# Optimization experiments

Measured on AMD Instinct MI355X. Metric: run time of the kernel, lower is better.

## Reference

```python
import jax, jax.numpy as jnp
import numpy as np
from jax import lax

B, T, R, D = 32, 128, 9, 512


def conv2d(x, w, b):
    # x: (N,C,H,W), w: (O,I,kh,kw)
    y = lax.conv_general_dilated(x, w, (1, 1), 'VALID', dimension_numbers=('NCHW', 'OIHW', 'NCHW'))
    return y + b[None, :, None, None]


def pad1(x):
    return jnp.pad(x, ((0, 0), (0, 0), (1, 1), (1, 1)))


def maxpool2(x):
    return lax.reduce_window(x, -jnp.inf, lax.max, (1, 1, 2, 2), (1, 1, 2, 2), 'VALID')


def f2f_similarity(q, t, qm, tm):
    # q,t: (B,T,R,D). Region-pairwise sims then Chamfer: max over target regions p (axis 3), mean over query regions o (axis 2).
    sim = jnp.einsum('biok,bjpk->biopj', q, t)   # (B,T,R,R,T) large intermediate
    sim = jnp.mean(jnp.max(sim, axis=3), axis=2)  # (B,T,T)
    smask = qm[:, :, None] * tm[:, None, :]       # (B,T,T)
    sim = jnp.where(smask > 0, sim, 0.0)
    return sim, smask


def visil_head(sim, mask, w1, b1, w2, b2, w3, b3, wf, bf):
    # ViSiL VideoComperator: zeropad1+conv3x3+relu+maxpool2 (x2), zeropad1+conv3x3+relu, 1x1 conv
    x = sim[:, None]   # (N,1,T,T)
    m = mask[:, None]
    x = maxpool2(jax.nn.relu(conv2d(pad1(x), w1, b1)))
    m = maxpool2(m)
    x = maxpool2(jax.nn.relu(conv2d(pad1(x), w2, b2)))
    m = maxpool2(m)
    x = jax.nn.relu(conv2d(pad1(x), w3, b3))
    x = conv2d(x, wf, bf)   # 1x1 conv -> 1 channel
    return x[:, 0], m[:, 0]


def chamfer_v2v(s, m):
    # masked Chamfer: max over axis 2, masked mean over axis 1
    s = jnp.where(m > 0, s, -jnp.inf)
    s = jnp.max(s, axis=2)
    mm = jnp.max(m, axis=2)
    s = jnp.where(mm > 0, s, 0.0)
    return jnp.sum(s, axis=1) / jnp.sum(mm, axis=1)


def setup_inputs():
    key = jax.random.key(0)
    ks = jax.random.split(key, 8)
    return {
        'anchors': jax.random.normal(ks[0], (B, T, R, D), jnp.float32),
        'positives': jax.random.normal(ks[1], (B, T, R, D), jnp.float32),
        'negatives': jax.random.normal(ks[2], (B, T, R, D), jnp.float32),
        'anchors_masks': jnp.ones((B, T), jnp.float32),
        'positive_masks': jnp.ones((B, T), jnp.float32),
        'negative_masks': jnp.ones((B, T), jnp.float32),
        'w1': jax.random.normal(ks[3], (32, 1, 3, 3), jnp.float32) * 0.05,
        'b1': jnp.zeros((32,), jnp.float32),
        'w2': jax.random.normal(ks[4], (64, 32, 3, 3), jnp.float32) * 0.05,
        'b2': jnp.zeros((64,), jnp.float32),
        'w3': jax.random.normal(ks[5], (128, 64, 3, 3), jnp.float32) * 0.05,
        'b3': jnp.zeros((128,), jnp.float32),
        'wf': jax.random.normal(ks[6], (1, 128, 1, 1), jnp.float32) * 0.05,
        'bf': jnp.zeros((1,), jnp.float32),
    }


def reference(anchors, positives, negatives, anchors_masks, positive_masks, negative_masks, w1, b1, w2, b2, w3, b3, wf, bf):
    pos_sim, pos_mask = f2f_similarity(anchors, positives, anchors_masks, positive_masks)
    neg_sim, neg_mask = f2f_similarity(anchors, negatives, anchors_masks, negative_masks)
    sim = jnp.concatenate([pos_sim, neg_sim], 0)
    smask = jnp.concatenate([pos_mask, neg_mask], 0)
    sim, smask = visil_head(sim, smask, w1, b1, w2, b2, w3, b3, wf, bf)
    # SimilarityRegularizationLoss(min_val=-1, max_val=1)
    loss = jnp.sum(jax.nn.relu(-1.0 - sim)) + jnp.sum(jax.nn.relu(sim - 1.0))
    sim = jnp.clip(sim, -1.0, 1.0)  # Hardtanh
    v2v = chamfer_v2v(sim, smask)   # (2B,)
    pos_pair, neg_pair = jnp.split(v2v[:, None], 2, axis=0)
    return pos_pair, neg_pair, loss
```

## Files before the change

### kernel.cpp

```cpp
#include <hip/hip_runtime.h>
#include <math.h>

#define BTRD (128*9*512)

typedef _Float16 half8 __attribute__((ext_vector_type(8)));
typedef float f32x4 __attribute__((ext_vector_type(4)));

__global__ __launch_bounds__(256) void prep_kernel(
    const float* __restrict__ P, const float* __restrict__ Nn,
    _Float16* __restrict__ Pf, _Float16* __restrict__ Nf,
    const float* __restrict__ w2, const float* __restrict__ w3,
    _Float16* __restrict__ w2t, _Float16* __restrict__ w3t)
{
  int bid = blockIdx.x;
  if (bid < 18432) {
    int which = bid / 9216;
    const float* in = which == 0 ? P : Nn;
    _Float16* out = which == 0 ? Pf : Nf;
    int idx = (bid - which * 9216) * 256 + threadIdx.x;
    const float4* in4 = (const float4*)in;
    float4 a = in4[idx * 2], c = in4[idx * 2 + 1];
    half8 h = { (_Float16)a.x, (_Float16)a.y, (_Float16)a.z, (_Float16)a.w,
                (_Float16)c.x, (_Float16)c.y, (_Float16)c.z, (_Float16)c.w };
    ((half8*)out)[idx] = h;
  } else {
    int idx = (bid - 18432) * 256 + threadIdx.x;
    if (idx < 18432) {
      int tap = idx >> 11, oc = (idx >> 5) & 63, ic = idx & 31;
      w2t[idx] = (_Float16)w2[(oc * 32 + ic) * 9 + tap];
    } else if (idx < 18432 + 73728) {
      int j = idx - 18432;
      int tap = j >> 13, oc = (j >> 6) & 127, ic = j & 63;
      w3t[j] = (_Float16)w3[(oc * 64 + ic) * 9 + tap];
    }
  }
}

template<int O, int OB>
__device__ __forceinline__ void sim_run(
    const float* __restrict__ Q32, const _Float16* __restrict__ T,
    _Float16* __restrict__ lds, int i0, int tid, int jhalf,
    int pb, int b, int g,
    const float* __restrict__ qm, const float* __restrict__ pm,
    const float* __restrict__ nm, float* __restrict__ simout)
{
  int lane = tid & 63;
  int lrow = lane & 15, lk8 = lane >> 4;
  _Float16* tb0 = lds + 73728;
  _Float16* tb1 = lds + 73728 + 4096;

  {
    const float* qb = Q32 + ((size_t)(i0 * 9) << 9);
    for (int it = 0; it < 36; it++) {
      int c = it * 256 + tid;
      int r = c >> 6, sp = c & 63;
      const float* src = qb + ((size_t)r << 9) + (sp << 3);
      float4 a = *(const float4*)src;
      float4 cc = *(const float4*)(src + 4);
      half8 h = { (_Float16)a.x, (_Float16)a.y, (_Float16)a.z, (_Float16)a.w,
                  (_Float16)cc.x, (_Float16)cc.y, (_Float16)cc.z, (_Float16)cc.w };
      *(half8*)&lds[r * 512 + ((sp ^ (r & 7)) << 3)] = h;
    }
  }

  int c0 = tid, c1 = tid + 256;
  int j0c = c0 >> 2, sp0 = c0 & 3;
  int j1c = c1 >> 2, sp1 = c1 & 3;
  const _Float16* tg0 = T + ((size_t)(j0c * 9) << 9) + (sp0 << 3);
  const _Float16* tg1 = T + ((size_t)(j1c * 9) << 9) + (sp1 << 3);
  int ld0 = j0c * 32 + ((sp0 ^ ((j0c >> 1) & 3)) << 3);
  int ld1 = j1c * 32 + ((sp1 ^ ((j1c >> 1) & 3)) << 3);

  half8 st[4][2];

#define T_ISSUE(SET, S) do {                                              \
    int _s = (S);                                                         \
    int _p = _s >> 4; _p = _p > 8 ? 8 : _p;                               \
    int _off = (_p << 9) + ((_s & 15) << 5);                              \
    st[SET][0] = *(const half8*)(tg0 + _off);                             \
    st[SET][1] = *(const half8*)(tg1 + _off);                             \
  } while (0)

#define T_WRITE(SET, PAR) do {                                            \
    _Float16* _buf = (PAR) ? tb1 : tb0;                                   \
    *(half8*)&_buf[ld0] = st[SET][0];                                     \
    *(half8*)&_buf[ld1] = st[SET][1];                                     \
  } while (0)

  T_ISSUE(0, 0);
  T_ISSUE(1, 1);
  T_ISSUE(2, 2);
  T_WRITE(0, 0);
  asm volatile("s_waitcnt lgkmcnt(0)" ::: "memory");
  __builtin_amdgcn_s_barrier();
  __builtin_amdgcn_sched_barrier(0);

  f32x4 acc[O][4], mx[O][4];
#pragma unroll
  for (int oo = 0; oo < O; oo++)
#pragma unroll
    for (int jt = 0; jt < 4; jt++) {
      acc[oo][jt] = (f32x4){0.f, 0.f, 0.f, 0.f};
      mx[oo][jt] = (f32x4){-INFINITY, -INFINITY, -INFINITY, -INFINITY};
    }

  for (int p = 0; p < 9; p++) {
#pragma unroll
    for (int kc = 0; kc < 16; kc++) {
      int s = p * 16 + kc;
      T_ISSUE((kc + 3) & 3, s + 3);
      T_WRITE((kc + 1) & 3, (kc + 1) & 1);

      const _Float16* cur = (kc & 1) ? tb1 : tb0;
      half8 bfr[4];
#pragma unroll
      for (int jt = 0; jt < 4; jt++) {
        int j = jhalf * 64 + jt * 16 + lrow;
        bfr[jt] = *(const half8*)&cur[j * 32 + ((lk8 ^ ((j >> 1) & 3)) << 3)];
      }
#pragma unroll
      for (int oo = 0; oo < O; oo++) {
        int r = lrow * 9 + OB + oo;
        half8 afr = *(const half8*)&lds[r * 512 + ((((kc << 2) + lk8) ^ (r & 7)) << 3)];
#pragma unroll
        for (int jt = 0; jt < 4; jt++)
          acc[oo][jt] = __builtin_amdgcn_mfma_f32_16x16x32_f16(afr, bfr[jt], acc[oo][jt], 0, 0, 0);
      }

      if (kc == 15) {
#pragma unroll
        for (int oo = 0; oo < O; oo++)
#pragma unroll
          for (int jt = 0; jt < 4; jt++) {
#pragma unroll
            for (int e = 0; e < 4; e++)
              mx[oo][jt][e] = fmaxf(mx[oo][jt][e], acc[oo][jt][e]);
            acc[oo][jt] = (f32x4){0.f, 0.f, 0.f, 0.f};
          }
      }
      asm volatile("s_waitcnt lgkmcnt(0)" ::: "memory");
      __builtin_amdgcn_s_barrier();
      __builtin_amdgcn_sched_barrier(0);
    }
  }
#undef T_ISSUE
#undef T_WRITE

  f32x4 ps[4];
#pragma unroll
  for (int jt = 0; jt < 4; jt++) {
    ps[jt] = mx[0][jt];
#pragma unroll
    for (int oo = 1; oo < O; oo++) ps[jt] += mx[oo][jt];
  }

  float* ex = (float*)(lds + 73728);
  if (OB != 0) {
#pragma unroll
    for (int jt = 0; jt < 4; jt++)
      *(f32x4*)&ex[((jt * 2 + jhalf) * 64 + lane) * 4] = ps[jt];
  }
  __syncthreads();
  if (OB == 0) {
    const float* tm = (g ? nm : pm) + b * 128;
    const float* qmv = qm + b * 128;
    const float inv9 = 1.0f / 9.0f;
#pragma unroll
    for (int jt = 0; jt < 4; jt++) {
      ps[jt] += *(const f32x4*)&ex[((jt * 2 + jhalf) * 64 + lane) * 4];
      int j = jhalf * 64 + jt * 16 + lrow;
      float tmv = tm[j];
#pragma unroll
      for (int e = 0; e < 4; e++) {
        int i = i0 + (lk8 << 2) + e;
        float m = qmv[i] * tmv;
        simout[((size_t)pb << 14) + (i << 7) + j] = (m > 0.f) ? ps[jt][e] * inv9 : 0.f;
      }
    }
  }
}

__global__ __launch_bounds__(256, 1) void sim_mfma_kernel(
    const float* __restrict__ A32, const _Float16* __restrict__ Pf,
    const _Float16* __restrict__ Nf,
    const float* __restrict__ qm, const float* __restrict__ pm,
    const float* __restrict__ nm, float* __restrict__ simout)
{
  __shared__ _Float16 lds[81920];

  int n = blockIdx.x;
  int xcd = n & 7, slot = n >> 3;
  int pb = xcd * 8 + (slot >> 3);
  int ib = slot & 7;
  int b = pb & 31, g = pb >> 5;
  const float* Q32 = A32 + (size_t)b * BTRD;
  const _Float16* T = (g ? Nf : Pf) + (size_t)b * BTRD;
  int i0 = ib * 16;

  int tid = threadIdx.x;
  int w = tid >> 6;
  int jhalf = w & 1;
  if ((w >> 1) == 0)
    sim_run<5, 0>(Q32, T, lds, i0, tid, jhalf, pb, b, g, qm, pm, nm, simout);
  else
    sim_run<4, 5>(Q32, T, lds, i0, tid, jhalf, pb, b, g, qm, pm, nm, simout);
}

__global__ __launch_bounds__(256) void conv1_kernel(
    const float* __restrict__ sim, const float* __restrict__ w1,
    const float* __restrict__ b1, _Float16* __restrict__ x1)
{
  __shared__ float w_s[288];
  __shared__ float b_s[32];
  int tid = threadIdx.x;
  for (int e = tid; e < 288; e += 256) w_s[e] = w1[e];
  if (tid < 32) b_s[tid] = b1[tid];
  __syncthreads();

  int idx = blockIdx.x * 256 + tid;
  int x = idx & 63, y = (idx >> 6) & 63, b2 = idx >> 12;
  const float* sb = sim + (size_t)b2 * 16384;

  float patch[4][4];
#pragma unroll
  for (int r = 0; r < 4; r++) {
    int Y = 2 * y - 1 + r;
#pragma unroll
    for (int c = 0; c < 4; c++) {
      int X = 2 * x - 1 + c;
      patch[r][c] = (Y >= 0 && Y < 128 && X >= 0 && X < 128) ? sb[Y * 128 + X] : 0.f;
    }
  }

  _Float16 vout[32];
#pragma unroll
  for (int oc = 0; oc < 32; oc++) {
    float c00 = 0, c01 = 0, c10 = 0, c11 = 0;
#pragma unroll
    for (int tap = 0; tap < 9; tap++) {
      int dy = tap / 3, dx = tap - dy * 3;
      float w = w_s[oc * 9 + tap];
      c00 = fmaf(w, patch[dy][dx], c00);
      c01 = fmaf(w, patch[dy][dx + 1], c01);
      c10 = fmaf(w, patch[dy + 1][dx], c10);
      c11 = fmaf(w, patch[dy + 1][dx + 1], c11);
    }
    float v = fmaxf(fmaxf(c00, c01), fmaxf(c10, c11)) + b_s[oc];
    vout[oc] = (_Float16)fmaxf(v, 0.f);
  }
  _Float16* dst = x1 + (((size_t)b2 * 64 + y) * 64 + x) * 32;
#pragma unroll
  for (int q = 0; q < 4; q++)
    *(half8*)(dst + q * 8) = *(half8*)&vout[q * 8];
}

__global__ __launch_bounds__(256, 2) void conv2_mfma(
    const _Float16* __restrict__ x1, const _Float16* __restrict__ w2t,
    const float* __restrict__ bb, _Float16* __restrict__ x2)
{
  __shared__ _Float16 in_s[4 * 6 * 66 * 8];
  __shared__ _Float16 w_s[9 * 64 * 40];
  __shared__ _Float16 pool_s[4][32 * 32];

  int b2 = blockIdx.y, ystrip = blockIdx.x;
  int y0 = ystrip * 4;
  int tid = threadIdx.x;
  int w = tid >> 6, lane = tid & 63;
  int wyp = w >> 1, wn = w & 1;
  int lrow = lane & 15, lk8 = lane >> 4;

  {
    int px = tid >> 2, seg = tid & 3;
    const _Float16* base = x1 + ((size_t)b2 * 64) * 64 * 32;
    for (int rr = 0; rr < 6; rr++) {
      int yy = y0 - 1 + rr;
      half8 v = {};
      if (yy >= 0 && yy < 64) v = *(const half8*)(base + ((size_t)yy * 64 + px) * 32 + seg * 8);
      *(half8*)&in_s[((seg * 6 + rr) * 66 + px + 1) * 8] = v;
    }
    if (tid < 48) {
      int pr = tid >> 1, side = tid & 1;
      *(half8*)&in_s[(pr * 66 + side * 65) * 8] = (half8){};
    }
  }
  for (int e = tid; e < 2304; e += 256)
    *(half8*)&w_s[(e >> 2) * 40 + (e & 3) * 8] = *(const half8*)&w2t[e * 8];
  __syncthreads();

  f32x4 acc[2][4][2];
#pragma unroll
  for (int yr = 0; yr < 2; yr++)
#pragma unroll
    for (int xt = 0; xt < 4; xt++)
#pragma unroll
      for (int nt = 0; nt < 2; nt++)
        acc[yr][xt][nt] = (f32x4){0.f, 0.f, 0.f, 0.f};

#pragma unroll
  for (int tap = 0; tap < 9; tap++) {
    int dy = tap / 3, dx = tap - dy * 3;
    half8 bfr[2];
#pragma unroll
    for (int nt = 0; nt < 2; nt++)
      bfr[nt] = *(const half8*)&w_s[(tap * 64 + wn * 32 + nt * 16 + lrow) * 40 + lk8 * 8];
#pragma unroll
    for (int yr = 0; yr < 2; yr++) {
      int rr = 2 * wyp + yr + dy;
#pragma unroll
      for (int xt = 0; xt < 4; xt++) {
        half8 afr = *(const half8*)&in_s[((lk8 * 6 + rr) * 66 + xt * 16 + lrow + dx) * 8];
#pragma unroll
        for (int nt = 0; nt < 2; nt++)
          acc[yr][xt][nt] = __builtin_amdgcn_mfma_f32_16x16x32_f16(afr, bfr[nt], acc[yr][xt][nt], 0, 0, 0);
      }
    }
  }

  float bbv[2] = { bb[wn * 32 + lrow], bb[wn * 32 + 16 + lrow] };
#pragma unroll
  for (int nt = 0; nt < 2; nt++)
#pragma unroll
    for (int xt = 0; xt < 4; xt++)
#pragma unroll
      for (int pe = 0; pe < 2; pe++) {
        float m = fmaxf(fmaxf(acc[0][xt][nt][2 * pe], acc[0][xt][nt][2 * pe + 1]),
                        fmaxf(acc[1][xt][nt][2 * pe], acc[1][xt][nt][2 * pe + 1]));
        float v = fmaxf(m + bbv[nt], 0.f);
        int px = xt * 8 + lk8 * 2 + pe;
        pool_s[w][px * 32 + nt * 16 + lrow] = (_Float16)v;
      }
  __syncthreads();

  {
    int py = ystrip * 2 + wyp;
    int px = lane & 31, half = lane >> 5;
    const _Float16* srcp = &pool_s[w][px * 32 + half * 16];
    _Float16* dst = x2 + (((size_t)b2 * 32 + py) * 32 + px) * 64 + wn * 32 + half * 16;
    *(half8*)dst = *(const half8*)srcp;
    *(half8*)(dst + 8) = *(const half8*)(srcp + 8);
  }
}

__global__ __launch_bounds__(256, 2) void conv3_mfma(
    const _Float16* __restrict__ x2, const _Float16* __restrict__ w3t,
    const float* __restrict__ b3, const float* __restrict__ wf,
    const float* __restrict__ bf, float* __restrict__ shead)
{
  __shared__ _Float16 in_s[8 * 6 * 34 * 8];
  __shared__ _Float16 w_s[9 * 32 * 72];

  int b2 = blockIdx.y, ystrip = blockIdx.x;
  int y0 = ystrip * 4;
  int tid = threadIdx.x, w = tid >> 6, lane = tid & 63;
  int lrow = lane & 15, lk8 = lane >> 4;

  {
    int px = tid >> 3, seg = tid & 7;
    const _Float16* base = x2 + ((size_t)b2 * 32) * 32 * 64;
    for (int rr = 0; rr < 6; rr++) {
      int yy = y0 - 1 + rr;
      half8 v = {};
      if (yy >= 0 && yy < 32) v = *(const half8*)(base + ((size_t)yy * 32 + px) * 64 + seg * 8);
      *(half8*)&in_s[((seg * 6 + rr) * 34 + px + 1) * 8] = v;
    }
    if (tid < 96) {
      int pr = tid >> 1, side = tid & 1;
      *(half8*)&in_s[(pr * 34 + side * 33) * 8] = (half8){};
    }
  }

  f32x4 spart[2];
  spart[0] = (f32x4){0.f, 0.f, 0.f, 0.f};
  spart[1] = (f32x4){0.f, 0.f, 0.f, 0.f};
  int y = y0 + w;

  for (int og = 0; og < 4; og++) {
    __syncthreads();
    for (int e = tid; e < 2304; e += 256) {
      int s = e & 7, o = (e >> 3) & 31, tap = e >> 8;
      *(half8*)&w_s[(tap * 32 + o) * 72 + s * 8] =
          *(const half8*)&w3t[((size_t)(tap * 128 + og * 32 + o)) * 64 + s * 8];
    }
    __syncthreads();

    f32x4 acc[2][2];
#pragma unroll
    for (int mt = 0; mt < 2; mt++)
#pragma unroll
      for (int nt = 0; nt < 2; nt++)
        acc[mt][nt] = (f32x4){0.f, 0.f, 0.f, 0.f};

#pragma unroll
    for (int tap = 0; tap < 9; tap++) {
      int dy = tap / 3, dx = tap - dy * 3;
#pragma unroll
      for (int kc = 0; kc < 2; kc++) {
        half8 bfr[2];
#pragma unroll
        for (int nt = 0; nt < 2; nt++)
          bfr[nt] = *(const half8*)&w_s[(tap * 32 + nt * 16 + lrow) * 72 + kc * 32 + lk8 * 8];
#pragma unroll
        for (int mt = 0; mt < 2; mt++) {
          half8 afr = *(const half8*)&in_s[(((kc * 4 + lk8) * 6 + w + dy) * 34 + mt * 16 + lrow + dx) * 8];
#pragma unroll
          for (int nt = 0; nt < 2; nt++)
            acc[mt][nt] = __builtin_amdgcn_mfma_f32_16x16x32_f16(afr, bfr[nt], acc[mt][nt], 0, 0, 0);
        }
      }
    }

#pragma unroll
    for (int nt = 0; nt < 2; nt++) {
      int oc = og * 32 + nt * 16 + lrow;
      float b3v = b3[oc], wfv = wf[oc];
#pragma unroll
      for (int mt = 0; mt < 2; mt++)
#pragma unroll
        for (int e = 0; e < 4; e++)
          spart[mt][e] = fmaf(fmaxf(acc[mt][nt][e] + b3v, 0.f), wfv, spart[mt][e]);
    }
  }

#pragma unroll
  for (int mt = 0; mt < 2; mt++)
#pragma unroll
    for (int e = 0; e < 4; e++) {
      float v = spart[mt][e];
      v += __shfl_xor(v, 1); v += __shfl_xor(v, 2);
      v += __shfl_xor(v, 4); v += __shfl_xor(v, 8);
      spart[mt][e] = v;
    }
  if (lrow == 0) {
    float bfv = bf[0];
#pragma unroll
    for (int mt = 0; mt < 2; mt++)
#pragma unroll
      for (int e = 0; e < 4; e++) {
        int x = mt * 16 + lk8 * 4 + e;
        shead[(size_t)b2 * 1024 + y * 32 + x] = spart[mt][e] + bfv;
      }
  }
}

__global__ __launch_bounds__(256) void head_final_kernel(
    const float* __restrict__ shead, const float* __restrict__ qm,
    const float* __restrict__ pm, const float* __restrict__ nm,
    float* __restrict__ out, float* __restrict__ loss_ws)
{
  int b2 = blockIdx.x, b = b2 & 31, g = b2 >> 5;
  const float* qmv = qm + b * 128;
  const float* tmv = (g ? nm : pm) + b * 128;

  __shared__ float mq4[32], mt4[32];
  __shared__ float red[256];
  __shared__ float rowv[32], rowm[32];

  int tid = threadIdx.x;
  if (tid < 32) {
    float a = qmv[tid * 4];
    a = fmaxf(a, qmv[tid * 4 + 1]); a = fmaxf(a, qmv[tid * 4 + 2]); a = fmaxf(a, qmv[tid * 4 + 3]);
    mq4[tid] = a;
    float c = tmv[tid * 4];
    c = fmaxf(c, tmv[tid * 4 + 1]); c = fmaxf(c, tmv[tid * 4 + 2]); c = fmaxf(c, tmv[tid * 4 + 3]);
    mt4[tid] = c;
  }
  __syncthreads();

  const float* s = shead + (size_t)b2 * 1024;
  float lp = 0.f;
#pragma unroll
  for (int r = 0; r < 4; r++) {
    float v = s[tid + 256 * r];
    lp += fmaxf(-1.f - v, 0.f) + fmaxf(v - 1.f, 0.f);
  }
  red[tid] = lp;
  __syncthreads();
  for (int off = 128; off; off >>= 1) {
    if (tid < off) red[tid] += red[tid + off];
    __syncthreads();
  }
  if (tid == 0) loss_ws[b2] = red[0];

  if (tid < 32) {
    int y = tid;
    float mqy = mq4[y];
    float rmax = -INFINITY, mm = 0.f;
    for (int x = 0; x < 32; x++) {
      float m = mqy * mt4[x];
      mm = fmaxf(mm, m);
      float v = s[y * 32 + x];
      v = fminf(fmaxf(v, -1.f), 1.f);
      rmax = fmaxf(rmax, m > 0.f ? v : -INFINITY);
    }
    rowv[y] = (mm > 0.f) ? rmax : 0.f;
    rowm[y] = mm;
  }
  __syncthreads();
  if (tid == 0) {
    float ss = 0.f, sm = 0.f;
    for (int y = 0; y < 32; y++) { ss += rowv[y]; sm += rowm[y]; }
    out[b2] = ss / sm;
  }
}

__global__ void loss_sum_kernel(const float* __restrict__ loss_ws, float* __restrict__ out)
{
  float v = loss_ws[threadIdx.x];
#pragma unroll
  for (int off = 32; off >= 1; off >>= 1) v += __shfl_down(v, off);
  if (threadIdx.x == 0) out[64] = v;
}

extern "C" void kernel_launch(void* const* d_in, const int* in_sizes, int n_in,
                              void* d_out, int out_size, void* d_ws, size_t ws_size,
                              hipStream_t stream)
{
  (void)in_sizes; (void)n_in; (void)out_size; (void)ws_size;
  const float* A   = (const float*)d_in[0];
  const float* P   = (const float*)d_in[1];
  const float* Nn  = (const float*)d_in[2];
  const float* qm  = (const float*)d_in[3];
  const float* pm  = (const float*)d_in[4];
  const float* nm  = (const float*)d_in[5];
  const float* w1  = (const float*)d_in[6];
  const float* b1  = (const float*)d_in[7];
  const float* w2  = (const float*)d_in[8];
  const float* b2w = (const float*)d_in[9];
  const float* w3  = (const float*)d_in[10];
  const float* b3  = (const float*)d_in[11];
  const float* wf  = (const float*)d_in[12];
  const float* bf  = (const float*)d_in[13];
  float* out = (float*)d_out;

  const size_t F16SZ = (size_t)BTRD * 32 * sizeof(_Float16);
  char* ws = (char*)d_ws;
  _Float16* Pf = (_Float16*)(ws);
  _Float16* Nf = (_Float16*)(ws + F16SZ);
  char* ws2 = ws + 2 * F16SZ;
  float*     sim   = (float*)(ws2);
  _Float16*  x1    = (_Float16*)(ws2 + (4u << 20));
  _Float16*  x2    = (_Float16*)(ws2 + (20u << 20));
  float*     shead = (float*)(ws2 + (28u << 20));
  _Float16*  w2t   = (_Float16*)(ws2 + (29u << 20));
  _Float16*  w3t   = (_Float16*)(ws2 + (29u << 20) + (256u << 10));
  float*     lws   = (float*)(ws2 + (30u << 20));

  prep_kernel<<<18792, 256, 0, stream>>>(P, Nn, Pf, Nf, w2, w3, w2t, w3t);

  sim_mfma_kernel<<<512, 256, 0, stream>>>(A, Pf, Nf, qm, pm, nm, sim);
  conv1_kernel<<<1024, 256, 0, stream>>>(sim, w1, b1, x1);
  conv2_mfma<<<dim3(16, 64), 256, 0, stream>>>(x1, w2t, b2w, x2);
  conv3_mfma<<<dim3(8, 64), 256, 0, stream>>>(x2, w3t, b3, wf, bf, shead);
  head_final_kernel<<<64, 256, 0, stream>>>(shead, qm, pm, nm, out, lws);
  loss_sum_kernel<<<1, 64, 0, stream>>>(lws, out);
}
```

Before: 208.5 us.

## Share anchor tile across positive and negative passes, load target fragments directly

The similarity kernel now launches one block per (batch, query tile) with 512 threads. Each block converts the anchor tile to fp16 in LDS once and reuses it for both the positive and negative targets, instead of one block per target. Target fragments are loaded straight from global memory into registers with a small software prefetch ring, which removes the LDS staging buffers and the per-step barriers. This halves anchor conversion and LDS fill work and drops synchronisation, but it halves the grid to 256 blocks and relies on uncoalesced direct global reads of the target data.

```diff
diff --git a/kernel.cpp b/kernel.cpp
--- a/kernel.cpp
+++ b/kernel.cpp
@@ -38,21 +38,20 @@
 
 template<int O, int OB>
 __device__ __forceinline__ void sim_run(
-    const float* __restrict__ Q32, const _Float16* __restrict__ T,
-    _Float16* __restrict__ lds, int i0, int tid, int jhalf,
-    int pb, int b, int g,
+    const float* __restrict__ Q32, const _Float16* __restrict__ TP,
+    const _Float16* __restrict__ TN,
+    _Float16* __restrict__ lds, int i0, int tid, int jq, int b,
     const float* __restrict__ qm, const float* __restrict__ pm,
     const float* __restrict__ nm, float* __restrict__ simout)
 {
   int lane = tid & 63;
   int lrow = lane & 15, lk8 = lane >> 4;
-  _Float16* tb0 = lds + 73728;
-  _Float16* tb1 = lds + 73728 + 4096;
 
   {
     const float* qb = Q32 + ((size_t)(i0 * 9) << 9);
-    for (int it = 0; it < 36; it++) {
-      int c = it * 256 + tid;
+#pragma unroll
+    for (int it = 0; it < 18; it++) {
+      int c = it * 512 + tid;
       int r = c >> 6, sp = c & 63;
       const float* src = qb + ((size_t)r << 9) + (sp << 3);
       float4 a = *(const float4*)src;
@@ -62,148 +61,123 @@
       *(half8*)&lds[r * 512 + ((sp ^ (r & 7)) << 3)] = h;
     }
   }
-
-  int c0 = tid, c1 = tid + 256;
-  int j0c = c0 >> 2, sp0 = c0 & 3;
-  int j1c = c1 >> 2, sp1 = c1 & 3;
-  const _Float16* tg0 = T + ((size_t)(j0c * 9) << 9) + (sp0 << 3);
-  const _Float16* tg1 = T + ((size_t)(j1c * 9) << 9) + (sp1 << 3);
-  int ld0 = j0c * 32 + ((sp0 ^ ((j0c >> 1) & 3)) << 3);
-  int ld1 = j1c * 32 + ((sp1 ^ ((j1c >> 1) & 3)) << 3);
-
-  half8 st[4][2];
-
-#define T_ISSUE(SET, S) do {                                              \
-    int _s = (S);                                                         \
-    int _p = _s >> 4; _p = _p > 8 ? 8 : _p;                               \
-    int _off = (_p << 9) + ((_s & 15) << 5);                              \
-    st[SET][0] = *(const half8*)(tg0 + _off);                             \
-    st[SET][1] = *(const half8*)(tg1 + _off);                             \
-  } while (0)
-
-#define T_WRITE(SET, PAR) do {                                            \
-    _Float16* _buf = (PAR) ? tb1 : tb0;                                   \
-    *(half8*)&_buf[ld0] = st[SET][0];                                     \
-    *(half8*)&_buf[ld1] = st[SET][1];                                     \
-  } while (0)
-
-  T_ISSUE(0, 0);
-  T_ISSUE(1, 1);
-  T_ISSUE(2, 2);
-  T_WRITE(0, 0);
-  asm volatile("s_waitcnt lgkmcnt(0)" ::: "memory");
-  __builtin_amdgcn_s_barrier();
-  __builtin_amdgcn_sched_barrier(0);
-
-  f32x4 acc[O][4], mx[O][4];
-#pragma unroll
-  for (int oo = 0; oo < O; oo++)
-#pragma unroll
-    for (int jt = 0; jt < 4; jt++) {
-      acc[oo][jt] = (f32x4){0.f, 0.f, 0.f, 0.f};
-      mx[oo][jt] = (f32x4){-INFINITY, -INFINITY, -INFINITY, -INFINITY};
-    }
-
-  for (int p = 0; p < 9; p++) {
-#pragma unroll
-    for (int kc = 0; kc < 16; kc++) {
-      int s = p * 16 + kc;
-      T_ISSUE((kc + 3) & 3, s + 3);
-      T_WRITE((kc + 1) & 3, (kc + 1) & 1);
-
-      const _Float16* cur = (kc & 1) ? tb1 : tb0;
-      half8 bfr[4];
-#pragma unroll
-      for (int jt = 0; jt < 4; jt++) {
-        int j = jhalf * 64 + jt * 16 + lrow;
-        bfr[jt] = *(const half8*)&cur[j * 32 + ((lk8 ^ ((j >> 1) & 3)) << 3)];
-      }
-#pragma unroll
-      for (int oo = 0; oo < O; oo++) {
-        int r = lrow * 9 + OB + oo;
-        half8 afr = *(const half8*)&lds[r * 512 + ((((kc << 2) + lk8) ^ (r & 7)) << 3)];
-#pragma unroll
-        for (int jt = 0; jt < 4; jt++)
-          acc[oo][jt] = __builtin_amdgcn_mfma_f32_16x16x32_f16(afr, bfr[jt], acc[oo][jt], 0, 0, 0);
-      }
-
-      if (kc == 15) {
-#pragma unroll
-        for (int oo = 0; oo < O; oo++)
-#pragma unroll
-          for (int jt = 0; jt < 4; jt++) {
-#pragma unroll
-            for (int e = 0; e < 4; e++)
-              mx[oo][jt][e] = fmaxf(mx[oo][jt][e], acc[oo][jt][e]);
-            acc[oo][jt] = (f32x4){0.f, 0.f, 0.f, 0.f};
-          }
-      }
-      asm volatile("s_waitcnt lgkmcnt(0)" ::: "memory");
-      __builtin_amdgcn_s_barrier();
-      __builtin_amdgcn_sched_barrier(0);
-    }
-  }
-#undef T_ISSUE
-#undef T_WRITE
-
-  f32x4 ps[4];
-#pragma unroll
-  for (int jt = 0; jt < 4; jt++) {
-    ps[jt] = mx[0][jt];
-#pragma unroll
-    for (int oo = 1; oo < O; oo++) ps[jt] += mx[oo][jt];
-  }
+  __syncthreads();
 
   float* ex = (float*)(lds + 73728);
-  if (OB != 0) {
-#pragma unroll
-    for (int jt = 0; jt < 4; jt++)
-      *(f32x4*)&ex[((jt * 2 + jhalf) * 64 + lane) * 4] = ps[jt];
-  }
-  __syncthreads();
-  if (OB == 0) {
-    const float* tm = (g ? nm : pm) + b * 128;
-    const float* qmv = qm + b * 128;
-    const float inv9 = 1.0f / 9.0f;
-#pragma unroll
-    for (int jt = 0; jt < 4; jt++) {
-      ps[jt] += *(const f32x4*)&ex[((jt * 2 + jhalf) * 64 + lane) * 4];
-      int j = jhalf * 64 + jt * 16 + lrow;
-      float tmv = tm[j];
-#pragma unroll
-      for (int e = 0; e < 4; e++) {
-        int i = i0 + (lk8 << 2) + e;
-        float m = qmv[i] * tmv;
-        simout[((size_t)pb << 14) + (i << 7) + j] = (m > 0.f) ? ps[jt][e] * inv9 : 0.f;
-      }
-    }
-  }
-}
-
-__global__ __launch_bounds__(256, 1) void sim_mfma_kernel(
+  const float* qmv = qm + b * 128;
+  const float inv9 = 1.0f / 9.0f;
+
+  for (int tsel = 0; tsel < 2; ++tsel) {
+    const _Float16* T = tsel ? TN : TP;
+    const _Float16* tg0 = T + (size_t)(jq * 32 + lrow) * 4608 + (lk8 << 3);
+    const _Float16* tg1 = tg0 + (size_t)16 * 4608;
+
+    half8 Bb[4][2];
+    f32x4 acc[O][2], mx[O][2];
+#pragma unroll
+    for (int oo = 0; oo < O; oo++)
+#pragma unroll
+      for (int jt = 0; jt < 2; jt++) {
+        acc[oo][jt] = (f32x4){0.f, 0.f, 0.f, 0.f};
+        mx[oo][jt] = (f32x4){-INFINITY, -INFINITY, -INFINITY, -INFINITY};
+      }
+
+#define B_ISSUE(SET, S) do {                                              \
+      int _s = (S);                                                       \
+      int _p = _s >> 4; if (_p > 8) _p = 8;                               \
+      int _off = (_p << 9) + ((_s & 15) << 5);                            \
+      Bb[SET][0] = *(const half8*)(tg0 + _off);                           \
+      Bb[SET][1] = *(const half8*)(tg1 + _off);                           \
+    } while (0)
+
+    B_ISSUE(0, 0);
+    B_ISSUE(1, 1);
+
+    for (int p = 0; p < 9; ++p) {
+#pragma unroll
+      for (int kc = 0; kc < 16; ++kc) {
+        int s = p * 16 + kc;
+        B_ISSUE((kc + 2) & 3, s + 2);
+#pragma unroll
+        for (int oo = 0; oo < O; ++oo) {
+          int r = lrow * 9 + OB + oo;
+          half8 afr = *(const half8*)&lds[r * 512 + ((((kc << 2) + lk8) ^ (r & 7)) << 3)];
+          acc[oo][0] = __builtin_amdgcn_mfma_f32_16x16x32_f16(afr, Bb[kc & 3][0], acc[oo][0], 0, 0, 0);
+          acc[oo][1] = __builtin_amdgcn_mfma_f32_16x16x32_f16(afr, Bb[kc & 3][1], acc[oo][1], 0, 0, 0);
+        }
+        if (kc == 15) {
+#pragma unroll
+          for (int oo = 0; oo < O; oo++)
+#pragma unroll
+            for (int jt = 0; jt < 2; jt++) {
+#pragma unroll
+              for (int e = 0; e < 4; e++)
+                mx[oo][jt][e] = fmaxf(mx[oo][jt][e], acc[oo][jt][e]);
+              acc[oo][jt] = (f32x4){0.f, 0.f, 0.f, 0.f};
+            }
+        }
+      }
+    }
+#undef B_ISSUE
+
+    f32x4 ps[2];
+#pragma unroll
+    for (int jt = 0; jt < 2; jt++) {
+      ps[jt] = mx[0][jt];
+#pragma unroll
+      for (int oo = 1; oo < O; oo++) ps[jt] += mx[oo][jt];
+    }
+
+    if (OB != 0) {
+#pragma unroll
+      for (int jt = 0; jt < 2; jt++)
+        *(f32x4*)&ex[((jq * 64 + lane) * 2 + jt) * 4] = ps[jt];
+    }
+    __syncthreads();
+    if (OB == 0) {
+      const float* tm = (tsel ? nm : pm) + b * 128;
+      int pb = b + tsel * 32;
+#pragma unroll
+      for (int jt = 0; jt < 2; jt++) {
+        ps[jt] += *(const f32x4*)&ex[((jq * 64 + lane) * 2 + jt) * 4];
+        int j = jq * 32 + jt * 16 + lrow;
+        float tmv = tm[j];
+#pragma unroll
+        for (int e = 0; e < 4; e++) {
+          int i = i0 + (lk8 << 2) + e;
+          float m = qmv[i] * tmv;
+          simout[((size_t)pb << 14) + (i << 7) + j] = (m > 0.f) ? ps[jt][e] * inv9 : 0.f;
+        }
+      }
+    }
+    __syncthreads();
+  }
+}
+
+__global__ __launch_bounds__(512, 1) void sim_mfma_kernel(
     const float* __restrict__ A32, const _Float16* __restrict__ Pf,
     const _Float16* __restrict__ Nf,
     const float* __restrict__ qm, const float* __restrict__ pm,
     const float* __restrict__ nm, float* __restrict__ simout)
 {
-  __shared__ _Float16 lds[81920];
+  __shared__ _Float16 lds[73728 + 4096];
 
   int n = blockIdx.x;
   int xcd = n & 7, slot = n >> 3;
-  int pb = xcd * 8 + (slot >> 3);
+  int b = xcd * 4 + (slot >> 3);
   int ib = slot & 7;
-  int b = pb & 31, g = pb >> 5;
   const float* Q32 = A32 + (size_t)b * BTRD;
-  const _Float16* T = (g ? Nf : Pf) + (size_t)b * BTRD;
+  const _Float16* TP = Pf + (size_t)b * BTRD;
+  const _Float16* TN = Nf + (size_t)b * BTRD;
   int i0 = ib * 16;
 
   int tid = threadIdx.x;
   int w = tid >> 6;
-  int jhalf = w & 1;
-  if ((w >> 1) == 0)
-    sim_run<5, 0>(Q32, T, lds, i0, tid, jhalf, pb, b, g, qm, pm, nm, simout);
+  int jq = w & 3;
+  if ((w >> 2) == 0)
+    sim_run<5, 0>(Q32, TP, TN, lds, i0, tid, jq, b, qm, pm, nm, simout);
   else
-    sim_run<4, 5>(Q32, T, lds, i0, tid, jhalf, pb, b, g, qm, pm, nm, simout);
+    sim_run<4, 5>(Q32, TP, TN, lds, i0, tid, jq, b, qm, pm, nm, simout);
 }
 
 __global__ __launch_bounds__(256) void conv1_kernel(
@@ -547,7 +521,7 @@
 
   prep_kernel<<<18792, 256, 0, stream>>>(P, Nn, Pf, Nf, w2, w3, w2t, w3t);
 
-  sim_mfma_kernel<<<512, 256, 0, stream>>>(A, Pf, Nf, qm, pm, nm, sim);
+  sim_mfma_kernel<<<256, 512, 0, stream>>>(A, Pf, Nf, qm, pm, nm, sim);
   conv1_kernel<<<1024, 256, 0, stream>>>(sim, w1, b1, x1);
   conv2_mfma<<<dim3(16, 64), 256, 0, stream>>>(x1, w2t, b2w, x2);
   conv3_mfma<<<dim3(8, 64), 256, 0, stream>>>(x2, w3t, b3, wf, bf, shead);
```

Result: slower. 498.1 us, median of 2 (+138.9%).
